# Kernel optimization log

Hardware: AMD Instinct MI355X
Metric: run time of the kernel (lower is better)

Reference implementation:

```python
import jax, jax.numpy as jnp
import numpy as np

IN_CH, C_M, C_N = 512, 512, 128
B, H, W = 16, 56, 56


def setup_inputs() -> dict:
    key = jax.random.key(0)
    ks = jax.random.split(key, 7)
    s = 1.0 / np.sqrt(IN_CH)
    return {
        "x": jax.random.normal(ks[0], (B, IN_CH, H, W), dtype=jnp.float32),
        "wA": jax.random.uniform(ks[1], (C_M, IN_CH), jnp.float32, -s, s),
        "bA": jax.random.uniform(ks[2], (C_M,), jnp.float32, -s, s),
        "wB": jax.random.uniform(ks[3], (C_N, IN_CH), jnp.float32, -s, s),
        "bB": jax.random.uniform(ks[4], (C_N,), jnp.float32, -s, s),
        "wV": jax.random.uniform(ks[5], (C_N, IN_CH), jnp.float32, -s, s),
        "bV": jax.random.uniform(ks[6], (C_N,), jnp.float32, -s, s),
        "K": 1,
    }


def reference(x, wA, bA, wB, bB, wV, bV, K):
    b, c, h, w = x.shape
    c_m, c_n = wA.shape[0], wB.shape[0]
    batch = b // K
    hw = h * w
    N = K * hw
    # 1x1 convs == channel-wise matmuls
    A = jnp.einsum('bchw,mc->bmhw', x, wA) + bA[None, :, None, None]
    Bf = jnp.einsum('bchw,nc->bnhw', x, wB) + bB[None, :, None, None]
    Vf = jnp.einsum('bchw,nc->bnhw', x, wV) + bV[None, :, None, None]
    # (batch, c_m, K*h*w)
    tmpA = A.reshape(batch, K, c_m, hw).transpose(0, 2, 1, 3).reshape(batch, c_m, N)
    # softmax over the spatial dim N (torch Softmax() on 2D -> dim=1)
    tmpB = Bf.reshape(batch, K, c_n, hw).transpose(0, 2, 1, 3).reshape(batch, c_n, N)
    attB = jax.nn.softmax(tmpB, axis=-1).transpose(0, 2, 1)  # (batch, N, c_n)
    # softmax over channel dim c_n
    tmpV = Vf.reshape(batch, K, c_n, hw).transpose(0, 1, 3, 2).reshape(batch, N, c_n)
    attV = jax.nn.softmax(tmpV, axis=-1).transpose(0, 2, 1)  # (batch, c_n, N)
    G = jnp.matmul(tmpA, attB)   # (batch, c_m, c_n) global descriptors
    Z = jnp.matmul(G, attV)      # (batch, c_m, N) distribute
    Z = Z.reshape(batch, c_m, K, hw).transpose(0, 2, 1, 3).reshape(b, c_m, h, w)
    return Z
```

## Files before the change

kernel.cpp:

```cpp
#include <hip/hip_runtime.h>
#include <hip/hip_bf16.h>

#define BATCH 16
#define CIN   512
#define HW    3136
#define CM    512
#define CN    128
#define CBV   256

typedef short short8 __attribute__((ext_vector_type(8)));
typedef float f32x4  __attribute__((ext_vector_type(4)));

#define MFMA(a,b,c) __builtin_amdgcn_mfma_f32_16x16x32_bf16((a),(b),(c),0,0,0)

__device__ __forceinline__ void cvt_store8(__bf16* dst, const float* src) {
  const f32x4 a = *(const f32x4*)src;
  const f32x4 b = *(const f32x4*)(src + 4);
  __attribute__((aligned(16))) __bf16 t[8];
  t[0] = (__bf16)a[0]; t[1] = (__bf16)a[1]; t[2] = (__bf16)a[2]; t[3] = (__bf16)a[3];
  t[4] = (__bf16)b[0]; t[5] = (__bf16)b[1]; t[6] = (__bf16)b[2]; t[7] = (__bf16)b[3];
  *(uint4*)dst = *(uint4*)t;
}

__global__ __launch_bounds__(256) void wcast_kernel(
    const float* __restrict__ wB, const float* __restrict__ wV,
    const float* __restrict__ wA, __bf16* __restrict__ Wbf)
{
  size_t i = (size_t)blockIdx.x*2048 + (size_t)threadIdx.x*8;
  const float* src; size_t off;
  if (i < 65536)       { src = wB; off = i; }
  else if (i < 131072) { src = wV; off = i - 65536; }
  else                 { src = wA; off = i - 131072; }
  cvt_store8(Wbf + i, src + off);
}

__global__ __launch_bounds__(256) void transpose_x_kernel(
    const float* __restrict__ x, __bf16* __restrict__ xT)
{
  const int s0 = blockIdx.x * 64;
  const int c0 = blockIdx.y * 128;
  const int b  = blockIdx.z;
  const int tid = threadIdx.x;
  __shared__ __attribute__((aligned(16))) __bf16 T[64*136];

  const float* xb = x + ((size_t)b*CIN + c0)*HW + s0;
  const int colg = tid & 7;
  const int pr   = tid >> 3;

  #pragma unroll
  for (int p = 0; p < 2; ++p) {
    int c = (pr + 32*p) * 2;
    const float* r0 = xb + (size_t)c*HW + colg*8;
    const float* r1 = r0 + HW;
    f32x4 a0 = *(const f32x4*)r0, a1 = *(const f32x4*)(r0 + 4);
    f32x4 b0 = *(const f32x4*)r1, b1 = *(const f32x4*)(r1 + 4);
    float va[8] = {a0[0],a0[1],a0[2],a0[3],a1[0],a1[1],a1[2],a1[3]};
    float vb[8] = {b0[0],b0[1],b0[2],b0[3],b1[0],b1[1],b1[2],b1[3]};
    const int off = ((c >> 3) ^ colg) * 8 + (c & 7);
    #pragma unroll
    for (int j = 0; j < 8; ++j) {
      int s = colg*8 + j;
      __attribute__((aligned(4))) __bf16 pairv[2] = { (__bf16)va[j], (__bf16)vb[j] };
      *(unsigned int*)&T[s*136 + off] = *(unsigned int*)pairv;
    }
  }
  __syncthreads();

  __bf16* dst = xT + ((size_t)b*HW + s0)*CIN + c0;
  const int cg = tid & 15, sr = tid >> 4;
  #pragma unroll
  for (int p = 0; p < 4; ++p) {
    int row = sr + 16*p;
    int oct = cg ^ ((row >> 3) & 7);
    *(uint4*)&dst[(size_t)row*CIN + cg*8] = *(uint4*)&T[row*136 + oct*8];
  }
}

__global__ __launch_bounds__(256) void conv_bv_kernel(
    const __bf16* __restrict__ Wbf, const __bf16* __restrict__ xT,
    const float* __restrict__ bB, const float* __restrict__ bV,
    __bf16* __restrict__ BVB, __bf16* __restrict__ attVT)
{
  const int s0  = blockIdx.x * 64;
  const int b   = blockIdx.y;
  const int tid = threadIdx.x;
  const int lane = tid & 63, w = tid >> 6;
  const int l15  = lane & 15, q = lane >> 4;

  __shared__ __attribute__((aligned(16))) char smem[46080];
  __bf16* Wt = (__bf16*)smem;
  __bf16* Xt = (__bf16*)(smem + 36864);
  __bf16* T  = (__bf16*)smem;
  __shared__ float Vm[2][64];
  __shared__ float Vs[2][64];

  f32x4 acc[4][4] = {};
  const __bf16* xTb = xT + (size_t)b*HW*CIN;
  const int colg = tid & 7, row0 = tid >> 3;

  for (int k0 = 0; k0 < CIN; k0 += 64) {
    #pragma unroll
    for (int p = 0; p < 8; ++p) {
      int row = row0 + 32*p;
      *(uint4*)&Wt[row*72 + colg*8] = *(const uint4*)(Wbf + (size_t)row*CIN + k0 + colg*8);
    }
    #pragma unroll
    for (int p = 0; p < 2; ++p) {
      int row = row0 + 32*p;
      *(uint4*)&Xt[row*72 + colg*8] = *(const uint4*)(xTb + (size_t)(s0+row)*CIN + k0 + colg*8);
    }
    __syncthreads();
    #pragma unroll
    for (int kk = 0; kk < 2; ++kk) {
      short8 a[4], bb[4];
      #pragma unroll
      for (int mi = 0; mi < 4; ++mi)
        a[mi] = *(short8*)&Wt[(w*64 + mi*16 + l15)*72 + kk*32 + q*8];
      #pragma unroll
      for (int si = 0; si < 4; ++si)
        bb[si] = *(short8*)&Xt[(si*16 + l15)*72 + kk*32 + q*8];
      #pragma unroll
      for (int mi = 0; mi < 4; ++mi)
        #pragma unroll
        for (int si = 0; si < 4; ++si)
          acc[mi][si] = MFMA(a[mi], bb[si], acc[mi][si]);
    }
    __syncthreads();
  }

  float bias[4][4];
  #pragma unroll
  for (int mi = 0; mi < 4; ++mi)
    #pragma unroll
    for (int r = 0; r < 4; ++r) {
      int nch = w*64 + mi*16 + q*4 + r;
      bias[mi][r] = (nch < CN) ? bB[nch] : bV[nch - CN];
    }

  if (w < 2) {
    const size_t outb = (size_t)b * CN * HW;
    #pragma unroll
    for (int mi = 0; mi < 4; ++mi)
      #pragma unroll
      for (int si = 0; si < 4; ++si) {
        int s = s0 + si*16 + l15;
        #pragma unroll
        for (int r = 0; r < 4; ++r) {
          int nch = w*64 + mi*16 + q*4 + r;
          BVB[outb + (size_t)nch*HW + s] = (__bf16)(acc[mi][si][r] + bias[mi][r]);
        }
      }
  } else {
    #pragma unroll
    for (int si = 0; si < 4; ++si) {
      float m = -1e30f;
      #pragma unroll
      for (int mi = 0; mi < 4; ++mi)
        #pragma unroll
        for (int r = 0; r < 4; ++r)
          m = fmaxf(m, acc[mi][si][r] + bias[mi][r]);
      m = fmaxf(m, __shfl_xor(m, 16));
      m = fmaxf(m, __shfl_xor(m, 32));
      if (q == 0) Vm[w-2][si*16 + l15] = m;
    }
  }
  __syncthreads();
  if (w >= 2) {
    #pragma unroll
    for (int si = 0; si < 4; ++si) {
      int idx = si*16 + l15;
      float ms = fmaxf(Vm[0][idx], Vm[1][idx]);
      float ssum = 0.f;
      #pragma unroll
      for (int mi = 0; mi < 4; ++mi)
        #pragma unroll
        for (int r = 0; r < 4; ++r) {
          float e = __expf(acc[mi][si][r] + bias[mi][r] - ms);
          acc[mi][si][r] = e;
          ssum += e;
        }
      ssum += __shfl_xor(ssum, 16);
      ssum += __shfl_xor(ssum, 32);
      if (q == 0) Vs[w-2][idx] = ssum;
    }
  }
  __syncthreads();
  if (w >= 2) {
    #pragma unroll
    for (int si = 0; si < 4; ++si) {
      int idx = si*16 + l15;
      float inv = 1.0f / (Vs[0][idx] + Vs[1][idx]);
      #pragma unroll
      for (int mi = 0; mi < 4; ++mi)
        #pragma unroll
        for (int r = 0; r < 4; ++r) {
          int j = (w-2)*64 + mi*16 + q*4 + r;
          T[idx*136 + j] = (__bf16)(acc[mi][si][r] * inv);
        }
    }
  }
  __syncthreads();
  __bf16* dst = attVT + ((size_t)b*HW + s0)*CN;
  #pragma unroll
  for (int k = 0; k < 4; ++k) {
    int chunk = tid + 256*k;
    int row = chunk >> 4, oct = chunk & 15;
    *(uint4*)&dst[(size_t)row*CN + oct*8] = *(uint4*)&T[row*136 + oct*8];
  }
}

__global__ __launch_bounds__(256) void bstats_kernel(
    const __bf16* __restrict__ BVB, float* __restrict__ sm, float* __restrict__ sinv)
{
  const int row = blockIdx.x*4 + (threadIdx.x >> 6);
  const int lane = threadIdx.x & 63;
  const __bf16* rp = BVB + (size_t)row*HW;

  uint4 raw[7];
  float mx = -1e30f;
  #pragma unroll
  for (int i = 0; i < 6; ++i) {
    raw[i] = *(const uint4*)(rp + (lane + 64*i)*8);
    const __bf16* v = (const __bf16*)&raw[i];
    #pragma unroll
    for (int j = 0; j < 8; ++j) mx = fmaxf(mx, (float)v[j]);
  }
  if (lane < 8) {
    raw[6] = *(const uint4*)(rp + (lane + 384)*8);
    const __bf16* v = (const __bf16*)&raw[6];
    #pragma unroll
    for (int j = 0; j < 8; ++j) mx = fmaxf(mx, (float)v[j]);
  }
  #pragma unroll
  for (int off = 1; off < 64; off <<= 1) mx = fmaxf(mx, __shfl_xor(mx, off));

  float sum = 0.f;
  #pragma unroll
  for (int i = 0; i < 6; ++i) {
    const __bf16* v = (const __bf16*)&raw[i];
    #pragma unroll
    for (int j = 0; j < 8; ++j) sum += __expf((float)v[j] - mx);
  }
  if (lane < 8) {
    const __bf16* v = (const __bf16*)&raw[6];
    #pragma unroll
    for (int j = 0; j < 8; ++j) sum += __expf((float)v[j] - mx);
  }
  #pragma unroll
  for (int off = 1; off < 64; off <<= 1) sum += __shfl_xor(sum, off);

  if (lane == 0) { sm[row] = mx; sinv[row] = 1.0f / sum; }
}

__global__ __launch_bounds__(256) void h_gemm_kernel(
    const float* __restrict__ x, const __bf16* __restrict__ BVB,
    const float* __restrict__ sm, const float* __restrict__ sinv,
    float* __restrict__ H)
{
  const int c0 = blockIdx.x * 128, b = blockIdx.y, kc = blockIdx.z;
  const int tid = threadIdx.x, lane = tid & 63, w = tid >> 6;
  const int l15 = lane & 15, q = lane >> 4;

  __shared__ __attribute__((aligned(16))) __bf16 At[128*72];
  __shared__ __attribute__((aligned(16))) __bf16 Bt[128*72];
  f32x4 acc[8][2] = {};

  const float* xb = x + ((size_t)b*CIN + c0)*HW;
  const __bf16* ab = BVB + (size_t)b*CN*HW;
  const float* smb = sm + b*CN;
  const float* sib = sinv + b*CN;
  const int colg = tid & 7, row0 = tid >> 3;

  for (int ki = 0; ki < 7; ++ki) {
    int k0 = kc*448 + ki*64;
    #pragma unroll
    for (int p = 0; p < 4; ++p) {
      int row = row0 + 32*p;
      cvt_store8(&At[row*72 + colg*8], xb + (size_t)row*HW + k0 + colg*8);
    }
    #pragma unroll
    for (int p = 0; p < 4; ++p) {
      int row = row0 + 32*p;
      uint4 rawv = *(const uint4*)(ab + (size_t)row*HW + k0 + colg*8);
      const __bf16* v = (const __bf16*)&rawv;
      float mrow = smb[row], irow = sib[row];
      __attribute__((aligned(16))) __bf16 t[8];
      #pragma unroll
      for (int j = 0; j < 8; ++j)
        t[j] = (__bf16)(__expf((float)v[j] - mrow) * irow);
      *(uint4*)&Bt[row*72 + colg*8] = *(uint4*)t;
    }
    __syncthreads();
    #pragma unroll
    for (int kk = 0; kk < 2; ++kk) {
      short8 a[8], bb[2];
      #pragma unroll
      for (int mi = 0; mi < 8; ++mi)
        a[mi] = *(short8*)&At[(mi*16 + l15)*72 + kk*32 + q*8];
      #pragma unroll
      for (int ni = 0; ni < 2; ++ni)
        bb[ni] = *(short8*)&Bt[(w*32 + ni*16 + l15)*72 + kk*32 + q*8];
      #pragma unroll
      for (int mi = 0; mi < 8; ++mi)
        #pragma unroll
        for (int ni = 0; ni < 2; ++ni)
          acc[mi][ni] = MFMA(a[mi], bb[ni], acc[mi][ni]);
    }
    __syncthreads();
  }

  float* Hb = H + (size_t)b*CIN*CN;
  #pragma unroll
  for (int mi = 0; mi < 8; ++mi)
    #pragma unroll
    for (int ni = 0; ni < 2; ++ni)
      #pragma unroll
      for (int r = 0; r < 4; ++r) {
        int c = c0 + mi*16 + q*4 + r;
        int n = w*32 + ni*16 + l15;
        atomicAdd(&Hb[c*CN + n], acc[mi][ni][r]);
      }
}

__global__ __launch_bounds__(256) void g_gemm_kernel(
    const __bf16* __restrict__ wAbf, const float* __restrict__ bA,
    const float* __restrict__ H, __bf16* __restrict__ G)
{
  const int m0 = blockIdx.x * 64, b = blockIdx.y;
  const int tid = threadIdx.x, lane = tid & 63, w = tid >> 6;
  const int l15 = lane & 15, q = lane >> 4;

  __shared__ __attribute__((aligned(16))) __bf16 At[64*72];
  __shared__ __attribute__((aligned(16))) __bf16 Bt[128*72];
  f32x4 acc[4][2] = {};

  const float* Hb = H + (size_t)b*CIN*CN;
  const int colg = tid & 7, row0 = tid >> 3;
  const int nn = tid & 127, gh = tid >> 7;

  for (int k0 = 0; k0 < CIN; k0 += 64) {
    #pragma unroll
    for (int p = 0; p < 2; ++p) {
      int row = row0 + 32*p;
      *(uint4*)&At[row*72 + colg*8] = *(const uint4*)(wAbf + (size_t)(m0+row)*CIN + k0 + colg*8);
    }
    #pragma unroll
    for (int p = 0; p < 4; ++p) {
      int g = gh + 2*p;
      __attribute__((aligned(16))) __bf16 tmp[8];
      #pragma unroll
      for (int j = 0; j < 8; ++j)
        tmp[j] = (__bf16)Hb[(size_t)(k0 + g*8 + j)*CN + nn];
      *(uint4*)&Bt[nn*72 + g*8] = *(uint4*)tmp;
    }
    __syncthreads();
    #pragma unroll
    for (int kk = 0; kk < 2; ++kk) {
      short8 a[4], bb[2];
      #pragma unroll
      for (int mi = 0; mi < 4; ++mi)
        a[mi] = *(short8*)&At[(mi*16 + l15)*72 + kk*32 + q*8];
      #pragma unroll
      for (int ni = 0; ni < 2; ++ni)
        bb[ni] = *(short8*)&Bt[(w*32 + ni*16 + l15)*72 + kk*32 + q*8];
      #pragma unroll
      for (int mi = 0; mi < 4; ++mi)
        #pragma unroll
        for (int ni = 0; ni < 2; ++ni)
          acc[mi][ni] = MFMA(a[mi], bb[ni], acc[mi][ni]);
    }
    __syncthreads();
  }

  #pragma unroll
  for (int mi = 0; mi < 4; ++mi)
    #pragma unroll
    for (int ni = 0; ni < 2; ++ni)
      #pragma unroll
      for (int r = 0; r < 4; ++r) {
        int m = m0 + mi*16 + q*4 + r;
        int n = w*32 + ni*16 + l15;
        G[((size_t)b*CM + m)*CN + n] = (__bf16)(acc[mi][ni][r] + bA[m]);
      }
}

__global__ __launch_bounds__(256) void z_gemm_kernel(
    const __bf16* __restrict__ G, const __bf16* __restrict__ attVT,
    float* __restrict__ out)
{
  const int m0 = blockIdx.x * 128, s0 = blockIdx.y * 64, b = blockIdx.z;
  const int tid = threadIdx.x, lane = tid & 63, w = tid >> 6;
  const int l15 = lane & 15, q = lane >> 4;

  __shared__ __attribute__((aligned(16))) __bf16 At[128*136];
  __shared__ __attribute__((aligned(16))) __bf16 Bt[64*136];

  const __bf16* Gb = G + ((size_t)b*CM + m0)*CN;
  const __bf16* Vb = attVT + ((size_t)b*HW + s0)*CN;
  const int g = tid & 15, r0 = tid >> 4;
  #pragma unroll
  for (int p = 0; p < 8; ++p) {
    int row = r0 + 16*p;
    *(uint4*)&At[row*136 + g*8] = *(const uint4*)(Gb + (size_t)row*CN + g*8);
  }
  #pragma unroll
  for (int p = 0; p < 4; ++p) {
    int row = r0 + 16*p;
    *(uint4*)&Bt[row*136 + g*8] = *(const uint4*)(Vb + (size_t)row*CN + g*8);
  }
  __syncthreads();

  f32x4 acc[8] = {};
  #pragma unroll
  for (int kk = 0; kk < 4; ++kk) {
    short8 bb = *(short8*)&Bt[(w*16 + l15)*136 + kk*32 + q*8];
    #pragma unroll
    for (int mi = 0; mi < 8; ++mi) {
      short8 a = *(short8*)&At[(mi*16 + l15)*136 + kk*32 + q*8];
      acc[mi] = MFMA(a, bb, acc[mi]);
    }
  }

  const int s = s0 + w*16 + l15;
  #pragma unroll
  for (int mi = 0; mi < 8; ++mi)
    #pragma unroll
    for (int r = 0; r < 4; ++r) {
      int m = m0 + mi*16 + q*4 + r;
      out[((size_t)b*CM + m)*HW + s] = acc[mi][r];
    }
}

extern "C" void kernel_launch(void* const* d_in, const int* in_sizes, int n_in,
                              void* d_out, int out_size, void* d_ws, size_t ws_size,
                              hipStream_t stream)
{
  (void)in_sizes; (void)n_in; (void)out_size; (void)ws_size;
  const float* x  = (const float*)d_in[0];
  const float* wA = (const float*)d_in[1];
  const float* bA = (const float*)d_in[2];
  const float* wB = (const float*)d_in[3];
  const float* bB = (const float*)d_in[4];
  const float* wV = (const float*)d_in[5];
  const float* bV = (const float*)d_in[6];
  float* out = (float*)d_out;

  char* ws = (char*)d_ws;
  const size_t szXT    = (size_t)BATCH*HW*CIN*2;
  const size_t szWBF   = (size_t)(128*512 + 128*512 + 512*512)*2;
  const size_t szBVB   = (size_t)BATCH*CN*HW*2;
  const size_t szAttVT = (size_t)BATCH*HW*CN*2;
  const size_t szH     = (size_t)BATCH*CIN*CN*4;

  char* p = ws;
  __bf16* xT    = (__bf16*)p; p += szXT;
  __bf16* Wbf   = (__bf16*)p; p += szWBF;
  __bf16* BVB   = (__bf16*)p; p += szBVB;
  __bf16* attVT = (__bf16*)p; p += szAttVT;
  float*  H     = (float*)p;  p += szH;
  __bf16* G     = (__bf16*)p; p += (size_t)BATCH*CM*CN*2;
  float*  sm    = (float*)p;  p += (size_t)BATCH*CN*4;
  float*  sinv  = (float*)p;
  __bf16* wAbf  = Wbf + 2*128*512;

  wcast_kernel      <<<dim3(192),     256, 0, stream>>>(wB, wV, wA, Wbf);
  transpose_x_kernel<<<dim3(49,4,16), 256, 0, stream>>>(x, xT);
  conv_bv_kernel    <<<dim3(49,16),   256, 0, stream>>>(Wbf, xT, bB, bV, BVB, attVT);
  bstats_kernel     <<<dim3(512),     256, 0, stream>>>(BVB, sm, sinv);
  hipMemsetAsync(H, 0, szH, stream);
  h_gemm_kernel     <<<dim3(4,16,7),  256, 0, stream>>>(x, BVB, sm, sinv, H);
  g_gemm_kernel     <<<dim3(8,16),    256, 0, stream>>>(wAbf, bA, H, G);
  z_gemm_kernel     <<<dim3(4,49,16), 256, 0, stream>>>(G, attVT, out);
}
```

Measured before the change: 305.0 us.

## Fuse x transpose, weight cast and softmax stats into conv kernel

```diff
diff --git a/kernel.cpp b/kernel.cpp
--- a/kernel.cpp
+++ b/kernel.cpp
@@ -6,7 +6,6 @@
 #define HW    3136
 #define CM    512
 #define CN    128
-#define CBV   256
 
 typedef short short8 __attribute__((ext_vector_type(8)));
 typedef float f32x4  __attribute__((ext_vector_type(4)));
@@ -22,64 +21,12 @@
   *(uint4*)dst = *(uint4*)t;
 }
 
-__global__ __launch_bounds__(256) void wcast_kernel(
+__global__ __launch_bounds__(256) void conv_bv_kernel(
+    const float* __restrict__ x,
     const float* __restrict__ wB, const float* __restrict__ wV,
-    const float* __restrict__ wA, __bf16* __restrict__ Wbf)
-{
-  size_t i = (size_t)blockIdx.x*2048 + (size_t)threadIdx.x*8;
-  const float* src; size_t off;
-  if (i < 65536)       { src = wB; off = i; }
-  else if (i < 131072) { src = wV; off = i - 65536; }
-  else                 { src = wA; off = i - 131072; }
-  cvt_store8(Wbf + i, src + off);
-}
-
-__global__ __launch_bounds__(256) void transpose_x_kernel(
-    const float* __restrict__ x, __bf16* __restrict__ xT)
-{
-  const int s0 = blockIdx.x * 64;
-  const int c0 = blockIdx.y * 128;
-  const int b  = blockIdx.z;
-  const int tid = threadIdx.x;
-  __shared__ __attribute__((aligned(16))) __bf16 T[64*136];
-
-  const float* xb = x + ((size_t)b*CIN + c0)*HW + s0;
-  const int colg = tid & 7;
-  const int pr   = tid >> 3;
-
-  #pragma unroll
-  for (int p = 0; p < 2; ++p) {
-    int c = (pr + 32*p) * 2;
-    const float* r0 = xb + (size_t)c*HW + colg*8;
-    const float* r1 = r0 + HW;
-    f32x4 a0 = *(const f32x4*)r0, a1 = *(const f32x4*)(r0 + 4);
-    f32x4 b0 = *(const f32x4*)r1, b1 = *(const f32x4*)(r1 + 4);
-    float va[8] = {a0[0],a0[1],a0[2],a0[3],a1[0],a1[1],a1[2],a1[3]};
-    float vb[8] = {b0[0],b0[1],b0[2],b0[3],b1[0],b1[1],b1[2],b1[3]};
-    const int off = ((c >> 3) ^ colg) * 8 + (c & 7);
-    #pragma unroll
-    for (int j = 0; j < 8; ++j) {
-      int s = colg*8 + j;
-      __attribute__((aligned(4))) __bf16 pairv[2] = { (__bf16)va[j], (__bf16)vb[j] };
-      *(unsigned int*)&T[s*136 + off] = *(unsigned int*)pairv;
-    }
-  }
-  __syncthreads();
-
-  __bf16* dst = xT + ((size_t)b*HW + s0)*CIN + c0;
-  const int cg = tid & 15, sr = tid >> 4;
-  #pragma unroll
-  for (int p = 0; p < 4; ++p) {
-    int row = sr + 16*p;
-    int oct = cg ^ ((row >> 3) & 7);
-    *(uint4*)&dst[(size_t)row*CIN + cg*8] = *(uint4*)&T[row*136 + oct*8];
-  }
-}
-
-__global__ __launch_bounds__(256) void conv_bv_kernel(
-    const __bf16* __restrict__ Wbf, const __bf16* __restrict__ xT,
     const float* __restrict__ bB, const float* __restrict__ bV,
-    __bf16* __restrict__ BVB, __bf16* __restrict__ attVT)
+    __bf16* __restrict__ BVB, __bf16* __restrict__ attVT,
+    float* __restrict__ bsum)
 {
   const int s0  = blockIdx.x * 64;
   const int b   = blockIdx.y;
@@ -95,19 +42,31 @@
   __shared__ float Vs[2][64];
 
   f32x4 acc[4][4] = {};
-  const __bf16* xTb = xT + (size_t)b*HW*CIN;
+  const float* xb = x + (size_t)b*CIN*HW + s0;
   const int colg = tid & 7, row0 = tid >> 3;
+  const int cl = 2*(tid >> 3);
 
   for (int k0 = 0; k0 < CIN; k0 += 64) {
     #pragma unroll
     for (int p = 0; p < 8; ++p) {
       int row = row0 + 32*p;
-      *(uint4*)&Wt[row*72 + colg*8] = *(const uint4*)(Wbf + (size_t)row*CIN + k0 + colg*8);
-    }
-    #pragma unroll
-    for (int p = 0; p < 2; ++p) {
-      int row = row0 + 32*p;
-      *(uint4*)&Xt[row*72 + colg*8] = *(const uint4*)(xTb + (size_t)(s0+row)*CIN + k0 + colg*8);
+      const float* src = (row < 128) ? (wB + row*512) : (wV + (row-128)*512);
+      cvt_store8(&Wt[row*72 + colg*8], src + k0 + colg*8);
+    }
+    {
+      const float* r0 = xb + (size_t)(k0 + cl)*HW + colg*8;
+      const float* r1 = r0 + HW;
+      f32x4 a0 = *(const f32x4*)r0, a1 = *(const f32x4*)(r0 + 4);
+      f32x4 b0 = *(const f32x4*)r1, b1 = *(const f32x4*)(r1 + 4);
+      float va[8] = {a0[0],a0[1],a0[2],a0[3],a1[0],a1[1],a1[2],a1[3]};
+      float vb[8] = {b0[0],b0[1],b0[2],b0[3],b1[0],b1[1],b1[2],b1[3]};
+      const int off = ((cl >> 3) ^ colg)*8 + (cl & 7);
+      #pragma unroll
+      for (int j = 0; j < 8; ++j) {
+        int s = colg*8 + j;
+        __attribute__((aligned(4))) __bf16 pairv[2] = { (__bf16)va[j], (__bf16)vb[j] };
+        *(unsigned int*)&Xt[s*72 + off] = *(unsigned int*)pairv;
+      }
     }
     __syncthreads();
     #pragma unroll
@@ -117,8 +76,11 @@
       for (int mi = 0; mi < 4; ++mi)
         a[mi] = *(short8*)&Wt[(w*64 + mi*16 + l15)*72 + kk*32 + q*8];
       #pragma unroll
-      for (int si = 0; si < 4; ++si)
-        bb[si] = *(short8*)&Xt[(si*16 + l15)*72 + kk*32 + q*8];
+      for (int si = 0; si < 4; ++si) {
+        int s = si*16 + l15;
+        int oct = (kk*4 + q) ^ (si*2 + (l15 >> 3));
+        bb[si] = *(short8*)&Xt[s*72 + oct*8];
+      }
       #pragma unroll
       for (int mi = 0; mi < 4; ++mi)
         #pragma unroll
@@ -139,6 +101,7 @@
 
   if (w < 2) {
     const size_t outb = (size_t)b * CN * HW;
+    float psum[4][4] = {};
     #pragma unroll
     for (int mi = 0; mi < 4; ++mi)
       #pragma unroll
@@ -147,7 +110,21 @@
         #pragma unroll
         for (int r = 0; r < 4; ++r) {
           int nch = w*64 + mi*16 + q*4 + r;
-          BVB[outb + (size_t)nch*HW + s] = (__bf16)(acc[mi][si][r] + bias[mi][r]);
+          __bf16 bv = (__bf16)(acc[mi][si][r] + bias[mi][r]);
+          BVB[outb + (size_t)nch*HW + s] = bv;
+          psum[mi][r] += __expf((float)bv);
+        }
+      }
+    #pragma unroll
+    for (int mi = 0; mi < 4; ++mi)
+      #pragma unroll
+      for (int r = 0; r < 4; ++r) {
+        float v = psum[mi][r];
+        v += __shfl_xor(v, 1); v += __shfl_xor(v, 2);
+        v += __shfl_xor(v, 4); v += __shfl_xor(v, 8);
+        if (l15 == 0) {
+          int nch = w*64 + mi*16 + q*4 + r;
+          atomicAdd(&bsum[b*CN + nch], v);
         }
       }
   } else {
@@ -209,53 +186,9 @@
   }
 }
 
-__global__ __launch_bounds__(256) void bstats_kernel(
-    const __bf16* __restrict__ BVB, float* __restrict__ sm, float* __restrict__ sinv)
-{
-  const int row = blockIdx.x*4 + (threadIdx.x >> 6);
-  const int lane = threadIdx.x & 63;
-  const __bf16* rp = BVB + (size_t)row*HW;
-
-  uint4 raw[7];
-  float mx = -1e30f;
-  #pragma unroll
-  for (int i = 0; i < 6; ++i) {
-    raw[i] = *(const uint4*)(rp + (lane + 64*i)*8);
-    const __bf16* v = (const __bf16*)&raw[i];
-    #pragma unroll
-    for (int j = 0; j < 8; ++j) mx = fmaxf(mx, (float)v[j]);
-  }
-  if (lane < 8) {
-    raw[6] = *(const uint4*)(rp + (lane + 384)*8);
-    const __bf16* v = (const __bf16*)&raw[6];
-    #pragma unroll
-    for (int j = 0; j < 8; ++j) mx = fmaxf(mx, (float)v[j]);
-  }
-  #pragma unroll
-  for (int off = 1; off < 64; off <<= 1) mx = fmaxf(mx, __shfl_xor(mx, off));
-
-  float sum = 0.f;
-  #pragma unroll
-  for (int i = 0; i < 6; ++i) {
-    const __bf16* v = (const __bf16*)&raw[i];
-    #pragma unroll
-    for (int j = 0; j < 8; ++j) sum += __expf((float)v[j] - mx);
-  }
-  if (lane < 8) {
-    const __bf16* v = (const __bf16*)&raw[6];
-    #pragma unroll
-    for (int j = 0; j < 8; ++j) sum += __expf((float)v[j] - mx);
-  }
-  #pragma unroll
-  for (int off = 1; off < 64; off <<= 1) sum += __shfl_xor(sum, off);
-
-  if (lane == 0) { sm[row] = mx; sinv[row] = 1.0f / sum; }
-}
-
 __global__ __launch_bounds__(256) void h_gemm_kernel(
     const float* __restrict__ x, const __bf16* __restrict__ BVB,
-    const float* __restrict__ sm, const float* __restrict__ sinv,
-    float* __restrict__ H)
+    const float* __restrict__ bsum, float* __restrict__ H)
 {
   const int c0 = blockIdx.x * 128, b = blockIdx.y, kc = blockIdx.z;
   const int tid = threadIdx.x, lane = tid & 63, w = tid >> 6;
@@ -267,9 +200,12 @@
 
   const float* xb = x + ((size_t)b*CIN + c0)*HW;
   const __bf16* ab = BVB + (size_t)b*CN*HW;
-  const float* smb = sm + b*CN;
-  const float* sib = sinv + b*CN;
+  const float* bsb = bsum + b*CN;
   const int colg = tid & 7, row0 = tid >> 3;
+
+  float irow[4];
+  #pragma unroll
+  for (int p = 0; p < 4; ++p) irow[p] = 1.0f / bsb[row0 + 32*p];
 
   for (int ki = 0; ki < 7; ++ki) {
     int k0 = kc*448 + ki*64;
@@ -283,11 +219,10 @@
       int row = row0 + 32*p;
       uint4 rawv = *(const uint4*)(ab + (size_t)row*HW + k0 + colg*8);
       const __bf16* v = (const __bf16*)&rawv;
-      float mrow = smb[row], irow = sib[row];
       __attribute__((aligned(16))) __bf16 t[8];
       #pragma unroll
       for (int j = 0; j < 8; ++j)
-        t[j] = (__bf16)(__expf((float)v[j] - mrow) * irow);
+        t[j] = (__bf16)(__expf((float)v[j]) * irow[p]);
       *(uint4*)&Bt[row*72 + colg*8] = *(uint4*)t;
     }
     __syncthreads();
@@ -323,7 +258,7 @@
 }
 
 __global__ __launch_bounds__(256) void g_gemm_kernel(
-    const __bf16* __restrict__ wAbf, const float* __restrict__ bA,
+    const float* __restrict__ wA, const float* __restrict__ bA,
     const float* __restrict__ H, __bf16* __restrict__ G)
 {
   const int m0 = blockIdx.x * 64, b = blockIdx.y;
@@ -342,7 +277,7 @@
     #pragma unroll
     for (int p = 0; p < 2; ++p) {
       int row = row0 + 32*p;
-      *(uint4*)&At[row*72 + colg*8] = *(const uint4*)(wAbf + (size_t)(m0+row)*CIN + k0 + colg*8);
+      cvt_store8(&At[row*72 + colg*8], wA + (size_t)(m0+row)*CIN + k0 + colg*8);
     }
     #pragma unroll
     for (int p = 0; p < 4; ++p) {
@@ -446,29 +381,21 @@
   float* out = (float*)d_out;
 
   char* ws = (char*)d_ws;
-  const size_t szXT    = (size_t)BATCH*HW*CIN*2;
-  const size_t szWBF   = (size_t)(128*512 + 128*512 + 512*512)*2;
   const size_t szBVB   = (size_t)BATCH*CN*HW*2;
   const size_t szAttVT = (size_t)BATCH*HW*CN*2;
   const size_t szH     = (size_t)BATCH*CIN*CN*4;
+  const size_t szBsum  = (size_t)BATCH*CN*4;
 
   char* p = ws;
-  __bf16* xT    = (__bf16*)p; p += szXT;
-  __bf16* Wbf   = (__bf16*)p; p += szWBF;
   __bf16* BVB   = (__bf16*)p; p += szBVB;
   __bf16* attVT = (__bf16*)p; p += szAttVT;
   float*  H     = (float*)p;  p += szH;
-  __bf16* G     = (__bf16*)p; p += (size_t)BATCH*CM*CN*2;
-  float*  sm    = (float*)p;  p += (size_t)BATCH*CN*4;
-  float*  sinv  = (float*)p;
-  __bf16* wAbf  = Wbf + 2*128*512;
-
-  wcast_kernel      <<<dim3(192),     256, 0, stream>>>(wB, wV, wA, Wbf);
-  transpose_x_kernel<<<dim3(49,4,16), 256, 0, stream>>>(x, xT);
-  conv_bv_kernel    <<<dim3(49,16),   256, 0, stream>>>(Wbf, xT, bB, bV, BVB, attVT);
-  bstats_kernel     <<<dim3(512),     256, 0, stream>>>(BVB, sm, sinv);
-  hipMemsetAsync(H, 0, szH, stream);
-  h_gemm_kernel     <<<dim3(4,16,7),  256, 0, stream>>>(x, BVB, sm, sinv, H);
-  g_gemm_kernel     <<<dim3(8,16),    256, 0, stream>>>(wAbf, bA, H, G);
-  z_gemm_kernel     <<<dim3(4,49,16), 256, 0, stream>>>(G, attVT, out);
-}
+  float*  bsum  = (float*)p;  p += szBsum;
+  __bf16* G     = (__bf16*)p;
+
+  hipMemsetAsync(H, 0, szH + szBsum, stream);
+  conv_bv_kernel<<<dim3(49,16),   256, 0, stream>>>(x, wB, wV, bB, bV, BVB, attVT, bsum);
+  h_gemm_kernel <<<dim3(4,16,7),  256, 0, stream>>>(x, BVB, bsum, H);
+  g_gemm_kernel <<<dim3(8,16),    256, 0, stream>>>(wA, bA, H, G);
+  z_gemm_kernel <<<dim3(4,49,16), 256, 0, stream>>>(G, attVT, out);
+}
```

New measurement: 299.4 us. Within noise of the previous version (-1.8%).
